# Optimization experiments

Hardware: AMD Instinct MI355X
Metric: run time of the kernel (lower is better)

Reference implementation:

```python
import jax, jax.numpy as jnp
import numpy as np

B, S, D, R = 8, 512, 768, 128


def setup_inputs() -> dict:
    key = jax.random.key(0)
    k1, k2, k3 = jax.random.split(key, 3)
    embeddings = jax.random.normal(k1, (B, S, D), dtype=jnp.float32)
    # nn.init.uniform_(proj, -0.05, 0.05)
    proj_dist = jax.random.uniform(k2, (R, D), dtype=jnp.float32, minval=-0.05, maxval=0.05)
    proj_depth = jax.random.uniform(k3, (R, D), dtype=jnp.float32, minval=-0.05, maxval=0.05)
    return {"embeddings": embeddings, "proj_dist": proj_dist, "proj_depth": proj_depth}


def _distances(embeddings, proj):
    # (B,S,D) @ (D,R) -> (B,S,R)
    p = jnp.einsum('bsd,rd->bsr', embeddings, proj)
    # pairwise squared euclidean distances: sum_r (p_i - p_j)^2 -> (B,S,S)
    diff = p[:, :, None, :] - p[:, None, :, :]
    return jnp.sum(diff * diff, axis=-1)


def _depths(embeddings, proj):
    p = jnp.einsum('bsd,rd->bsr', embeddings, proj)
    return jnp.sum(p * p, axis=-1)  # (B,S)


def reference(embeddings, proj_dist, proj_depth):
    distances = _distances(embeddings, proj_dist)
    depths = _depths(embeddings, proj_depth)
    return (distances, depths)
```

## Files before the change

### kernel.cpp

```cpp
#include <hip/hip_runtime.h>

#define NB 8
#define NS 512
#define ND 768
#define NR 128
#define NM (NB * NS)
#define DIST_ELEMS ((size_t)NB * NS * NS)

typedef short bf16x8 __attribute__((ext_vector_type(8)));
typedef float f32x4  __attribute__((ext_vector_type(4)));

__device__ __forceinline__ unsigned short f2bf(float f) {
  unsigned int u = __float_as_uint(f);
  return (unsigned short)((u + 0x7FFFu + ((u >> 16) & 1u)) >> 16);
}
__device__ __forceinline__ float bf2f(unsigned short h) {
  return __uint_as_float(((unsigned int)h) << 16);
}

constexpr int KT = 32;

__global__ __launch_bounds__(256) void proj_kernel(
    const float* __restrict__ emb,
    const float* __restrict__ projD,
    const float* __restrict__ projP,
    unsigned short* __restrict__ P,
    float* __restrict__ normsD,
    float* __restrict__ depths)
{
  __shared__ unsigned short sA[64][KT];
  __shared__ unsigned short sB[64][KT];

  const int tid = threadIdx.x;
  const int ct  = blockIdx.x;
  const bool isDepth = (ct >= 2);
  const int n0  = (ct & 1) * 64;
  const int m0  = blockIdx.y * 64;
  const float* proj = (isDepth ? projP : projD) + (size_t)n0 * ND;

  const int srow = tid >> 2;
  const int skq  = tid & 3;
  const float* aRow = emb  + (size_t)(m0 + srow) * ND + skq * 8;
  const float* bRow = proj + (size_t)srow * ND + skq * 8;

  float4 a0 = *(const float4*)(aRow);
  float4 a1 = *(const float4*)(aRow + 4);
  float4 b0 = *(const float4*)(bRow);
  float4 b1 = *(const float4*)(bRow + 4);

  const int lane = tid & 63;
  const int w    = tid >> 6;
  const int ln   = lane & 15;
  const int q    = lane >> 4;

  f32x4 acc[4] = {};

  for (int kt = 0; kt < ND; kt += KT) {
    bf16x8 pa, pb;
    pa[0] = f2bf(a0.x); pa[1] = f2bf(a0.y); pa[2] = f2bf(a0.z); pa[3] = f2bf(a0.w);
    pa[4] = f2bf(a1.x); pa[5] = f2bf(a1.y); pa[6] = f2bf(a1.z); pa[7] = f2bf(a1.w);
    pb[0] = f2bf(b0.x); pb[1] = f2bf(b0.y); pb[2] = f2bf(b0.z); pb[3] = f2bf(b0.w);
    pb[4] = f2bf(b1.x); pb[5] = f2bf(b1.y); pb[6] = f2bf(b1.z); pb[7] = f2bf(b1.w);
    *(bf16x8*)(&sA[srow][skq * 8]) = pa;
    *(bf16x8*)(&sB[srow][skq * 8]) = pb;
    __syncthreads();
    if (kt + KT < ND) {
      a0 = *(const float4*)(aRow + kt + KT);
      a1 = *(const float4*)(aRow + kt + KT + 4);
      b0 = *(const float4*)(bRow + kt + KT);
      b1 = *(const float4*)(bRow + kt + KT + 4);
    }
    bf16x8 bq = *(const bf16x8*)(&sB[16 * w + ln][q * 8]);
    #pragma unroll
    for (int i = 0; i < 4; ++i) {
      bf16x8 aq = *(const bf16x8*)(&sA[16 * i + ln][q * 8]);
      acc[i] = __builtin_amdgcn_mfma_f32_16x16x32_bf16(aq, bq, acc[i], 0, 0, 0);
    }
    __syncthreads();
  }

  const int nG = n0 + 16 * w + ln;
  float* target = isDepth ? depths : normsD;
  #pragma unroll
  for (int i = 0; i < 4; ++i) {
    float vs[4];
    #pragma unroll
    for (int r = 0; r < 4; ++r) {
      unsigned short hb = f2bf(acc[i][r]);
      if (!isDepth)
        P[(size_t)(m0 + 16 * i + 4 * q + r) * NR + nG] = hb;
      float v = bf2f(hb);
      vs[r] = v * v;
    }
    #pragma unroll
    for (int r = 0; r < 4; ++r) {
      float s = vs[r];
      s += __shfl_xor(s, 1);
      s += __shfl_xor(s, 2);
      s += __shfl_xor(s, 4);
      s += __shfl_xor(s, 8);
      if (ln == 0) atomicAdd(&target[m0 + 16 * i + 4 * q + r], s);
    }
  }
}

__global__ __launch_bounds__(256) void dist_kernel(
    const unsigned short* __restrict__ P,
    const float* __restrict__ normsD,
    float* __restrict__ out)
{
  __shared__ unsigned short sPi[64][136];
  __shared__ unsigned short sPj[64][136];
  __shared__ float nIs[64], nJs[64];

  const int tid = threadIdx.x;
  const int b  = blockIdx.z;
  const int i0 = blockIdx.y * 64;
  const int j0 = blockIdx.x * 64;
  const unsigned short* Pb = P + (size_t)b * NS * NR;
  const float* normsB = normsD + (size_t)b * NS;

  const int grow = tid >> 4;
  const int gg   = tid & 15;
  #pragma unroll
  for (int jj = 0; jj < 4; ++jj) {
    const int row = grow + jj * 16;
    float4 vi = *(const float4*)(Pb + (size_t)(i0 + row) * NR + gg * 8);
    float4 vj = *(const float4*)(Pb + (size_t)(j0 + row) * NR + gg * 8);
    *(float4*)(&sPi[row][gg * 8]) = vi;
    *(float4*)(&sPj[row][gg * 8]) = vj;
  }
  if (tid < 64)       nIs[tid]      = normsB[i0 + tid];
  else if (tid < 128) nJs[tid - 64] = normsB[j0 + tid - 64];
  __syncthreads();

  const int lane = tid & 63;
  const int w    = tid >> 6;
  const int ln   = lane & 15;
  const int q    = lane >> 4;

  f32x4 acc[4] = {};
  #pragma unroll
  for (int ks = 0; ks < 4; ++ks) {
    bf16x8 bq = *(const bf16x8*)(&sPj[16 * w + ln][ks * 32 + q * 8]);
    #pragma unroll
    for (int i = 0; i < 4; ++i) {
      bf16x8 aq = *(const bf16x8*)(&sPi[16 * i + ln][ks * 32 + q * 8]);
      acc[i] = __builtin_amdgcn_mfma_f32_16x16x32_bf16(aq, bq, acc[i], 0, 0, 0);
    }
  }

  const int col = j0 + 16 * w + ln;
  const float nj = nJs[16 * w + ln];
  float* ob = out + (size_t)b * NS * NS;
  #pragma unroll
  for (int i = 0; i < 4; ++i) {
    #pragma unroll
    for (int r = 0; r < 4; ++r) {
      const int rloc = 16 * i + 4 * q + r;
      ob[(size_t)(i0 + rloc) * NS + col] = nIs[rloc] + nj - 2.0f * acc[i][r];
    }
  }
}

extern "C" void kernel_launch(void* const* d_in, const int* in_sizes, int n_in,
                              void* d_out, int out_size, void* d_ws, size_t ws_size,
                              hipStream_t stream) {
  const float* emb   = (const float*)d_in[0];
  const float* projD = (const float*)d_in[1];
  const float* projP = (const float*)d_in[2];
  float* out = (float*)d_out;

  unsigned short* P = (unsigned short*)d_ws;
  float* normsD = (float*)((char*)d_ws + (size_t)NM * NR * 2);
  float* depths = out + DIST_ELEMS;

  hipMemsetAsync(normsD, 0, NM * sizeof(float), stream);
  hipMemsetAsync(depths, 0, NM * sizeof(float), stream);

  proj_kernel<<<dim3(4, NM / 64), 256, 0, stream>>>(emb, projD, projP, P, normsD, depths);
  dist_kernel<<<dim3(NS / 64, NS / 64, NB), 256, 0, stream>>>(P, normsD, out);
}
```

Baseline: 88.68 us.

## Drop memsets and atomics; recompute dist norms in dist kernel, reduce depth in-block

The projection kernel now uses 32-row M tiles. Each depth block covers all 128 R columns, so the depth sum is reduced in shared memory and written directly, with no atomics or memsets. The separate normsD buffer is removed, and the distance kernel recomputes each row's squared norm from the bf16 P tile already in LDS. This removes two memset launches and global atomic traffic. In exchange, the depth blocks carry double the MFMA work, so load is unbalanced across the grid, and the distance kernel gains an extra sync and a small reduction pass.

```diff
diff --git a/kernel.cpp b/kernel.cpp
--- a/kernel.cpp
+++ b/kernel.cpp
@@ -17,6 +17,14 @@
 __device__ __forceinline__ float bf2f(unsigned short h) {
   return __uint_as_float(((unsigned int)h) << 16);
 }
+__device__ __forceinline__ bf16x8 pack8(float4 lo, float4 hi) {
+  bf16x8 p;
+  p[0] = (short)f2bf(lo.x); p[1] = (short)f2bf(lo.y);
+  p[2] = (short)f2bf(lo.z); p[3] = (short)f2bf(lo.w);
+  p[4] = (short)f2bf(hi.x); p[5] = (short)f2bf(hi.y);
+  p[6] = (short)f2bf(hi.z); p[7] = (short)f2bf(hi.w);
+  return p;
+}
 
 constexpr int KT = 32;
 
@@ -25,88 +33,101 @@
     const float* __restrict__ projD,
     const float* __restrict__ projP,
     unsigned short* __restrict__ P,
-    float* __restrict__ normsD,
     float* __restrict__ depths)
 {
-  __shared__ unsigned short sA[64][KT];
-  __shared__ unsigned short sB[64][KT];
+  __shared__ unsigned short sA[32][KT];
+  __shared__ unsigned short sB[128][KT];
+  __shared__ float sRed[4][32];
 
   const int tid = threadIdx.x;
   const int ct  = blockIdx.x;
-  const bool isDepth = (ct >= 2);
-  const int n0  = (ct & 1) * 64;
-  const int m0  = blockIdx.y * 64;
-  const float* proj = (isDepth ? projP : projD) + (size_t)n0 * ND;
-
-  const int srow = tid >> 2;
-  const int skq  = tid & 3;
-  const float* aRow = emb  + (size_t)(m0 + srow) * ND + skq * 8;
-  const float* bRow = proj + (size_t)srow * ND + skq * 8;
-
-  float4 a0 = *(const float4*)(aRow);
-  float4 a1 = *(const float4*)(aRow + 4);
-  float4 b0 = *(const float4*)(bRow);
-  float4 b1 = *(const float4*)(bRow + 4);
+  const bool isDepth = (ct == 2);
+  const int m0  = blockIdx.y * 32;
+  const float* proj = isDepth ? projP : (projD + (size_t)(ct * 64) * ND);
+
+  const int arow = tid >> 2;
+  const int aoct = tid & 3;
+  const float* aPtr = emb + (size_t)(m0 + (arow & 31)) * ND + aoct * 8;
+  const int brow0 = tid >> 2;
+  const int boct  = tid & 3;
+  const float* bPtr0 = proj + (size_t)brow0 * ND + boct * 8;
+  const float* bPtr1 = proj + (size_t)(brow0 + 64) * ND + boct * 8;
+
+  float4 a0, a1, b00, b01, b10, b11;
+  if (tid < 128) { a0 = *(const float4*)aPtr; a1 = *(const float4*)(aPtr + 4); }
+  b00 = *(const float4*)bPtr0; b01 = *(const float4*)(bPtr0 + 4);
+  if (isDepth) { b10 = *(const float4*)bPtr1; b11 = *(const float4*)(bPtr1 + 4); }
 
   const int lane = tid & 63;
   const int w    = tid >> 6;
   const int ln   = lane & 15;
   const int q    = lane >> 4;
 
-  f32x4 acc[4] = {};
+  f32x4 acc[2][2] = {};
 
   for (int kt = 0; kt < ND; kt += KT) {
-    bf16x8 pa, pb;
-    pa[0] = f2bf(a0.x); pa[1] = f2bf(a0.y); pa[2] = f2bf(a0.z); pa[3] = f2bf(a0.w);
-    pa[4] = f2bf(a1.x); pa[5] = f2bf(a1.y); pa[6] = f2bf(a1.z); pa[7] = f2bf(a1.w);
-    pb[0] = f2bf(b0.x); pb[1] = f2bf(b0.y); pb[2] = f2bf(b0.z); pb[3] = f2bf(b0.w);
-    pb[4] = f2bf(b1.x); pb[5] = f2bf(b1.y); pb[6] = f2bf(b1.z); pb[7] = f2bf(b1.w);
-    *(bf16x8*)(&sA[srow][skq * 8]) = pa;
-    *(bf16x8*)(&sB[srow][skq * 8]) = pb;
+    if (tid < 128) *(bf16x8*)(&sA[arow & 31][aoct * 8]) = pack8(a0, a1);
+    *(bf16x8*)(&sB[brow0][boct * 8]) = pack8(b00, b01);
+    if (isDepth) *(bf16x8*)(&sB[brow0 + 64][boct * 8]) = pack8(b10, b11);
     __syncthreads();
     if (kt + KT < ND) {
-      a0 = *(const float4*)(aRow + kt + KT);
-      a1 = *(const float4*)(aRow + kt + KT + 4);
-      b0 = *(const float4*)(bRow + kt + KT);
-      b1 = *(const float4*)(bRow + kt + KT + 4);
-    }
-    bf16x8 bq = *(const bf16x8*)(&sB[16 * w + ln][q * 8]);
-    #pragma unroll
-    for (int i = 0; i < 4; ++i) {
-      bf16x8 aq = *(const bf16x8*)(&sA[16 * i + ln][q * 8]);
-      acc[i] = __builtin_amdgcn_mfma_f32_16x16x32_bf16(aq, bq, acc[i], 0, 0, 0);
+      if (tid < 128) {
+        a0 = *(const float4*)(aPtr + kt + KT);
+        a1 = *(const float4*)(aPtr + kt + KT + 4);
+      }
+      b00 = *(const float4*)(bPtr0 + kt + KT);
+      b01 = *(const float4*)(bPtr0 + kt + KT + 4);
+      if (isDepth) {
+        b10 = *(const float4*)(bPtr1 + kt + KT);
+        b11 = *(const float4*)(bPtr1 + kt + KT + 4);
+      }
+    }
+    bf16x8 bq0 = *(const bf16x8*)(&sB[16 * w + ln][q * 8]);
+    if (!isDepth) {
+      #pragma unroll
+      for (int i = 0; i < 2; ++i) {
+        bf16x8 aq = *(const bf16x8*)(&sA[16 * i + ln][q * 8]);
+        acc[0][i] = __builtin_amdgcn_mfma_f32_16x16x32_bf16(aq, bq0, acc[0][i], 0, 0, 0);
+      }
+    } else {
+      bf16x8 bq1 = *(const bf16x8*)(&sB[64 + 16 * w + ln][q * 8]);
+      #pragma unroll
+      for (int i = 0; i < 2; ++i) {
+        bf16x8 aq = *(const bf16x8*)(&sA[16 * i + ln][q * 8]);
+        acc[0][i] = __builtin_amdgcn_mfma_f32_16x16x32_bf16(aq, bq0, acc[0][i], 0, 0, 0);
+        acc[1][i] = __builtin_amdgcn_mfma_f32_16x16x32_bf16(aq, bq1, acc[1][i], 0, 0, 0);
+      }
     }
     __syncthreads();
   }
 
-  const int nG = n0 + 16 * w + ln;
-  float* target = isDepth ? depths : normsD;
-  #pragma unroll
-  for (int i = 0; i < 4; ++i) {
-    float vs[4];
-    #pragma unroll
-    for (int r = 0; r < 4; ++r) {
-      unsigned short hb = f2bf(acc[i][r]);
-      if (!isDepth)
-        P[(size_t)(m0 + 16 * i + 4 * q + r) * NR + nG] = hb;
-      float v = bf2f(hb);
-      vs[r] = v * v;
-    }
-    #pragma unroll
-    for (int r = 0; r < 4; ++r) {
-      float s = vs[r];
-      s += __shfl_xor(s, 1);
-      s += __shfl_xor(s, 2);
-      s += __shfl_xor(s, 4);
-      s += __shfl_xor(s, 8);
-      if (ln == 0) atomicAdd(&target[m0 + 16 * i + 4 * q + r], s);
-    }
+  if (!isDepth) {
+    const int nG = ct * 64 + 16 * w + ln;
+    #pragma unroll
+    for (int i = 0; i < 2; ++i)
+      #pragma unroll
+      for (int r = 0; r < 4; ++r)
+        P[(size_t)(m0 + 16 * i + 4 * q + r) * NR + nG] = f2bf(acc[0][i][r]);
+  } else {
+    #pragma unroll
+    for (int i = 0; i < 2; ++i)
+      #pragma unroll
+      for (int r = 0; r < 4; ++r) {
+        float s = acc[0][i][r] * acc[0][i][r] + acc[1][i][r] * acc[1][i][r];
+        s += __shfl_xor(s, 1);
+        s += __shfl_xor(s, 2);
+        s += __shfl_xor(s, 4);
+        s += __shfl_xor(s, 8);
+        if (ln == 0) sRed[w][16 * i + 4 * q + r] = s;
+      }
+    __syncthreads();
+    if (tid < 32)
+      depths[m0 + tid] = sRed[0][tid] + sRed[1][tid] + sRed[2][tid] + sRed[3][tid];
   }
 }
 
 __global__ __launch_bounds__(256) void dist_kernel(
     const unsigned short* __restrict__ P,
-    const float* __restrict__ normsD,
     float* __restrict__ out)
 {
   __shared__ unsigned short sPi[64][136];
@@ -118,7 +139,6 @@
   const int i0 = blockIdx.y * 64;
   const int j0 = blockIdx.x * 64;
   const unsigned short* Pb = P + (size_t)b * NS * NR;
-  const float* normsB = normsD + (size_t)b * NS;
 
   const int grow = tid >> 4;
   const int gg   = tid & 15;
@@ -130,8 +150,26 @@
     *(float4*)(&sPi[row][gg * 8]) = vi;
     *(float4*)(&sPj[row][gg * 8]) = vj;
   }
-  if (tid < 64)       nIs[tid]      = normsB[i0 + tid];
-  else if (tid < 128) nJs[tid - 64] = normsB[j0 + tid - 64];
+  __syncthreads();
+
+  {
+    const int half = tid & 1;
+    const int row  = (tid >> 1) & 63;
+    const unsigned short* sp = (tid < 128) ? &sPi[row][half * 64]
+                                           : &sPj[row][half * 64];
+    float s = 0.f;
+    #pragma unroll
+    for (int g = 0; g < 8; ++g) {
+      bf16x8 v = *(const bf16x8*)(sp + g * 8);
+      #pragma unroll
+      for (int e = 0; e < 8; ++e) {
+        float f = bf2f((unsigned short)v[e]);
+        s += f * f;
+      }
+    }
+    s += __shfl_xor(s, 1);
+    if (half == 0) { if (tid < 128) nIs[row] = s; else nJs[row] = s; }
+  }
   __syncthreads();
 
   const int lane = tid & 63;
@@ -172,12 +210,8 @@
   float* out = (float*)d_out;
 
   unsigned short* P = (unsigned short*)d_ws;
-  float* normsD = (float*)((char*)d_ws + (size_t)NM * NR * 2);
   float* depths = out + DIST_ELEMS;
 
-  hipMemsetAsync(normsD, 0, NM * sizeof(float), stream);
-  hipMemsetAsync(depths, 0, NM * sizeof(float), stream);
-
-  proj_kernel<<<dim3(4, NM / 64), 256, 0, stream>>>(emb, projD, projP, P, normsD, depths);
-  dist_kernel<<<dim3(NS / 64, NS / 64, NB), 256, 0, stream>>>(P, normsD, out);
-}
+  proj_kernel<<<dim3(3, NM / 32), 256, 0, stream>>>(emb, projD, projP, P, depths);
+  dist_kernel<<<dim3(NS / 64, NS / 64, NB), 256, 0, stream>>>(P, out);
+}
```

Result: faster. 85.62 us (-3.4%).
